# Performance work log

Hardware: AMD Instinct MI355X
Metric: run time of the kernel (lower is better)

Reference implementation:

```python
import jax, jax.numpy as jnp
import numpy as np

VOCAB, EMB, FEAT = 30000, 300, 2048
B, NQ, NW, NK = 256, 32, 12, 64


def setup_inputs() -> dict:
    key = jax.random.key(0)
    ks = jax.random.split(key, 10)
    return {
        "wv": jax.random.normal(ks[0], (VOCAB, EMB), jnp.float32),
        "Wf": jax.random.normal(ks[1], (EMB, FEAT), jnp.float32) * 0.02,
        "bf": jax.random.normal(ks[2], (EMB,), jnp.float32) * 0.02,
        "Wp": jax.random.normal(ks[3], (EMB, EMB), jnp.float32) * 0.05,
        "bp": jax.random.normal(ks[4], (EMB,), jnp.float32) * 0.02,
        "Wm": jax.random.normal(ks[5], (EMB, EMB), jnp.float32) * 0.05,
        "bm": jax.random.normal(ks[6], (EMB,), jnp.float32) * 0.02,
        "feature": jax.random.normal(ks[7], (B, NK, FEAT), jnp.float32),
        "query": jax.random.randint(ks[8], (B, NQ, NW), 0, VOCAB),
        "label": jax.random.randint(ks[9], (B, NK), 0, VOCAB),
    }


def reference(wv, Wf, bf, Wp, bp, Wm, bm, feature, query, label):
    # Dropouts act as identity in eval mode.
    eps = 1e-5
    q_emb = wv[query]                                   # [B, queries, words, D]
    k_emb = wv[label] + feature @ Wf.T + bf             # [B, objects, D]
    scale = 1.0 / np.sqrt(EMB)
    att = jnp.einsum('byqd,bkd->byqk', q_emb, k_emb) * scale
    att = jax.nn.softmax(att, axis=-1)                  # over objects
    q_max_att = jnp.max(att, axis=3)                    # [B, queries, words]
    neg_inf = -jnp.finfo(q_max_att.dtype).max
    q_max_att = jnp.where(query == 0, neg_inf, q_max_att)
    q_max_norm_att = jax.nn.softmax(q_max_att, axis=-1) / 5.0
    p_emb = jnp.einsum('byq,byqd->byd', q_max_norm_att, q_emb)  # [B, queries, D]
    p_emb = (p_emb @ Wp.T + bp) + eps * (p_emb @ Wm.T + bm)
    return p_emb, k_emb
```

## Files before the change

kernel.cpp:

```cpp
#include <hip/hip_runtime.h>

typedef unsigned short u16;
typedef unsigned int u32;
typedef __bf16 bf16x8 __attribute__((ext_vector_type(8)));
typedef float f32x4 __attribute__((ext_vector_type(4)));

#if defined(__has_builtin)
#  if __has_builtin(__builtin_amdgcn_cvt_pk_bf16_f32)
#    define PK_BF16 1
#  endif
#endif

__device__ __forceinline__ u16 f2bu(float f){
  u32 u = __float_as_uint(f);
  return (u16)((u + 0x7fffu + ((u >> 16) & 1u)) >> 16);
}
__device__ __forceinline__ float b2f(u16 u){
  union { float f; u32 i; } v; v.i = ((u32)u) << 16; return v.f;
}
__device__ __forceinline__ u32 pkbf(float a, float b){
#ifdef PK_BF16
  typedef __bf16 bf16x2 __attribute__((ext_vector_type(2)));
  union { bf16x2 h; u32 u; } c;
  c.h = __builtin_amdgcn_cvt_pk_bf16_f32(a, b);
  return c.u;
#else
  return (u32)f2bu(a) | ((u32)f2bu(b) << 16);
#endif
}
__device__ __forceinline__ void glds16(const u16* g, u16* l){
  __builtin_amdgcn_global_load_lds(
      (const __attribute__((address_space(1))) void*)g,
      (__attribute__((address_space(3))) void*)l, 16, 0, 0);
}
__device__ __forceinline__ void glds16f(const float* g, float* l){
  __builtin_amdgcn_global_load_lds(
      (const __attribute__((address_space(1))) void*)g,
      (__attribute__((address_space(3))) void*)l, 16, 0, 0);
}

__global__ __launch_bounds__(256) void prep_wc(
    const float* __restrict__ Wp, const float* __restrict__ bp,
    const float* __restrict__ Wm, const float* __restrict__ bm,
    u16* __restrict__ Wc, float* __restrict__ bc)
{
  int idx = blockIdx.x * 256 + threadIdx.x;
  if (idx < 384 * 160) {
    int n = idx / 160, k = (idx % 160) * 2;
    float v0 = 0.f, v1 = 0.f;
    if (n < 300 && k < 300) {
      v0 = Wp[n * 300 + k]     + 1e-5f * Wm[n * 300 + k];
      v1 = Wp[n * 300 + k + 1] + 1e-5f * Wm[n * 300 + k + 1];
    }
    ((u32*)Wc)[idx] = pkbf(v0, v1);
    if (idx < 384) bc[idx] = (idx < 300) ? bp[idx] + 1e-5f * bm[idx] : 0.f;
  }
}

__global__ __launch_bounds__(256) void prep_wv16(
    const float* __restrict__ wv, u16* __restrict__ wv16)
{
  int idx = blockIdx.x * 256 + threadIdx.x;
  if (idx < 30000 * 160) {
    int row = idx / 160, k = (idx % 160) * 2;
    float v0 = 0.f, v1 = 0.f;
    if (k < 300) {
      v0 = wv[(size_t)row * 300 + k];
      v1 = wv[(size_t)row * 300 + k + 1];
    }
    ((u32*)wv16)[idx] = pkbf(v0, v1);
  }
}

__global__ __launch_bounds__(256) void prep_wf16(
    const float* __restrict__ Wf, u16* __restrict__ Wf16)
{
  int i = blockIdx.x * 256 + threadIdx.x;
  if (i < 384 * 1024) {
    int row = i >> 10, c2 = (i & 1023) * 2;
    float v0 = 0.f, v1 = 0.f;
    if (row < 300) {
      v0 = Wf[(size_t)row * 2048 + c2];
      v1 = Wf[(size_t)row * 2048 + c2 + 1];
    }
    ((u32*)Wf16)[i] = pkbf(v0, v1);
  }
}

template <int GLDS>
__global__ __launch_bounds__(256) void gemm0_kernel(
    const float* __restrict__ A, const float* __restrict__ B,
    const u16* __restrict__ Af16, const u16* __restrict__ Bf16,
    const float* __restrict__ bias,
    const int* __restrict__ label, const float* __restrict__ wv,
    float* __restrict__ C, u16* __restrict__ kemb16)
{
  __shared__ __align__(16) u16 As[128 * 32];
  __shared__ __align__(16) u16 Bs[128 * 32];
  const int lda = 2048, K = 2048, nbn = 3, nsrc = 300;
  int t = threadIdx.x;
  int bm = (blockIdx.x / nbn) * 128;
  int bn = (blockIdx.x % nbn) * 128;
  int lane = t & 63, w = t >> 6;
  int wm = (w >> 1) * 64, wn = (w & 1) * 64;

  f32x4 acc[4][4];
  for (int i = 0; i < 4; i++)
    for (int j = 0; j < 4; j++)
      for (int r = 0; r < 4; r++) acc[i][j][r] = 0.f;

  int mrow = lane & 15, q = lane >> 4;

  for (int kk = 0; kk < K; kk += 32) {
    #pragma unroll
    for (int p = 0; p < 2; p++) {
      int idx = t + p * 256;
      int row = idx >> 2, ch = idx & 3;
      int brow = bn + row;
      if (brow >= nsrc) brow = 0;
      const float4* ap = (const float4*)&A[(size_t)(bm + row) * lda + kk + ch * 8];
      float4 a0 = ap[0], a1 = ap[1];
      const float4* bpp = (const float4*)&B[(size_t)brow * lda + kk + ch * 8];
      float4 b0 = bpp[0], b1 = bpp[1];
      union { u32 u[4]; uint4 v; } pa, pb;
      pa.u[0] = pkbf(a0.x, a0.y); pa.u[1] = pkbf(a0.z, a0.w);
      pa.u[2] = pkbf(a1.x, a1.y); pa.u[3] = pkbf(a1.z, a1.w);
      pb.u[0] = pkbf(b0.x, b0.y); pb.u[1] = pkbf(b0.z, b0.w);
      pb.u[2] = pkbf(b1.x, b1.y); pb.u[3] = pkbf(b1.z, b1.w);
      *(uint4*)&As[idx * 8] = pa.v;
      *(uint4*)&Bs[idx * 8] = pb.v;
    }
    __syncthreads();

    bf16x8 af[4], bfr[4];
    #pragma unroll
    for (int i = 0; i < 4; i++)
      af[i] = *(const bf16x8*)&As[(wm + i * 16 + mrow) * 32 + q * 8];
    #pragma unroll
    for (int j = 0; j < 4; j++)
      bfr[j] = *(const bf16x8*)&Bs[(wn + j * 16 + mrow) * 32 + q * 8];
    #pragma unroll
    for (int i = 0; i < 4; i++)
      #pragma unroll
      for (int j = 0; j < 4; j++)
        acc[i][j] = __builtin_amdgcn_mfma_f32_16x16x32_bf16(
            af[i], bfr[j], acc[i][j], 0, 0, 0);
    __syncthreads();
  }

  #pragma unroll
  for (int i = 0; i < 4; i++)
    #pragma unroll
    for (int j = 0; j < 4; j++) {
      int col = bn + wn + j * 16 + (lane & 15);
      int rb = bm + wm + i * 16 + (lane >> 4) * 4;
      #pragma unroll
      for (int r = 0; r < 4; r++) {
        int m = rb + r;
        if (col < 300) {
          float v = acc[i][j][r];
          v += bias[col] + wv[(size_t)label[m] * 300 + col];
          C[(size_t)m * 300 + col] = v;
          if (kemb16) kemb16[(size_t)m * 320 + col] = f2bu(v);
        } else if (kemb16 && col < 320) {
          kemb16[(size_t)m * 320 + col] = 0;
        }
      }
    }
}

__global__ __launch_bounds__(64) void gemm0v5_kernel(
    const float* __restrict__ A, const u16* __restrict__ Bf16,
    const float* __restrict__ bias, const int* __restrict__ label,
    const float* __restrict__ wv, float* __restrict__ C,
    u16* __restrict__ kemb16)
{
  __shared__ __align__(16) float As[2][64 * 32];
  __shared__ __align__(16) u16  Bs[2][64 * 32];
  int lane = threadIdx.x;
  int g = blockIdx.x;
  int xcd = g & 7, loc = g >> 3;
  int mloc = loc / 5, nn = loc % 5;
  int bm = (xcd * 32 + mloc) * 64;
  int bn = nn * 64;
  int mrow = lane & 15, q = lane >> 4;

  f32x4 acc[4][4];
  #pragma unroll
  for (int i = 0; i < 4; i++)
    #pragma unroll
    for (int j = 0; j < 4; j++)
      #pragma unroll
      for (int r = 0; r < 4; r++) acc[i][j][r] = 0.f;

  int rlA = lane >> 3, chA = lane & 7;
  int rlB = lane >> 2, chB = lane & 3;
  const float* gA = &A[(size_t)(bm + rlA) * 2048 + ((chA ^ rlA) << 2)];
  const u16*   gB = &Bf16[(size_t)(bn + rlB) * 2048 + (chB << 3)];

#define STAGE_V5(buf, kk) do {                                          \
    _Pragma("unroll")                                                   \
    for (int p = 0; p < 8; p++)                                         \
      glds16f(gA + (size_t)p * 8 * 2048 + (kk), &As[buf][(p * 8) * 32]);\
    _Pragma("unroll")                                                   \
    for (int p = 0; p < 4; p++)                                         \
      glds16(gB + (size_t)p * 16 * 2048 + (kk), &Bs[buf][(p * 16) * 32]);\
  } while (0)

  STAGE_V5(0, 0);

  for (int it = 0; it < 64; ++it) {
    int cur = it & 1;
    if (it < 63) {
      STAGE_V5(cur ^ 1, (it + 1) * 32);
      asm volatile("s_waitcnt vmcnt(12)" ::: "memory");
    } else {
      asm volatile("s_waitcnt vmcnt(0)" ::: "memory");
    }
    __builtin_amdgcn_sched_barrier(0);

    bf16x8 af[4], bfr[4];
    #pragma unroll
    for (int i = 0; i < 4; i++) {
      int r = i * 16 + mrow;
      int c0 = ((2 * q) ^ (r & 7)) * 4;
      int c1 = ((2 * q + 1) ^ (r & 7)) * 4;
      f32x4 x = *(const f32x4*)&As[cur][r * 32 + c0];
      f32x4 y = *(const f32x4*)&As[cur][r * 32 + c1];
      union { u32 u[4]; bf16x8 h; } cc;
      cc.u[0] = pkbf(x[0], x[1]); cc.u[1] = pkbf(x[2], x[3]);
      cc.u[2] = pkbf(y[0], y[1]); cc.u[3] = pkbf(y[2], y[3]);
      af[i] = cc.h;
    }
    #pragma unroll
    for (int j = 0; j < 4; j++)
      bfr[j] = *(const bf16x8*)&Bs[cur][(j * 16 + mrow) * 32 + q * 8];
    #pragma unroll
    for (int i = 0; i < 4; i++)
      #pragma unroll
      for (int j = 0; j < 4; j++)
        acc[i][j] = __builtin_amdgcn_mfma_f32_16x16x32_bf16(
            af[i], bfr[j], acc[i][j], 0, 0, 0);
  }
#undef STAGE_V5

  #pragma unroll
  for (int i = 0; i < 4; i++)
    #pragma unroll
    for (int j = 0; j < 4; j++) {
      int col = bn + j * 16 + (lane & 15);
      int rb = bm + i * 16 + (lane >> 4) * 4;
      #pragma unroll
      for (int r = 0; r < 4; r++) {
        int m = rb + r;
        if (col < 300) {
          float v = acc[i][j][r] + bias[col] + wv[(size_t)label[m] * 300 + col];
          C[(size_t)m * 300 + col] = v;
          kemb16[(size_t)m * 320 + col] = f2bu(v);
        } else {
          kemb16[(size_t)m * 320 + col] = 0;
        }
      }
    }
}

#define KES 344
template <int FULL>
__global__ __launch_bounds__(256) void attn_kernel(
    const float* __restrict__ wv, const u16* __restrict__ wv16,
    const int* __restrict__ query,
    const float* __restrict__ kout, const u16* __restrict__ kemb16,
    u16* __restrict__ praw)
{
  __shared__ __align__(16) u16 ke[64 * KES];
  __shared__ __align__(16) int qoff[192];
  __shared__ __align__(16) float awd[192];
  __shared__ __align__(16) float wt[192];

  int blk = blockIdx.x, b = blk >> 1, bh = blk & 1;
  int t = threadIdx.x;
  int lane = t & 63, w = t >> 6;

  if (FULL) {
    for (int i = t; i < 2560; i += 256) {
      int row = i / 40, ch = i % 40;
      *(uint4*)&ke[row * KES + ch * 8] =
          *(const uint4*)&kemb16[(size_t)(b * 64 + row) * 320 + ch * 8];
    }
  } else {
    for (int i = t; i < 4800; i += 256) {
      int row = i / 75, c4 = i % 75;
      float4 v = *(const float4*)&kout[(size_t)(b * 64 + row) * 300 + c4 * 4];
      *(u32*)&ke[row * KES + c4 * 4]     = pkbf(v.x, v.y);
      *(u32*)&ke[row * KES + c4 * 4 + 2] = pkbf(v.z, v.w);
    }
    for (int i = t; i < 640; i += 256) {
      int row = i / 10, c2 = i % 10;
      *(u32*)&ke[row * KES + 300 + c2 * 2] = 0;
    }
  }
  if (t < 192)
    qoff[t] = query[b * 384 + bh * 192 + t] * (FULL ? 320 : 300);
  __syncthreads();

  int mrow = lane & 15, q = lane >> 4;
  f32x4 acc[3][4];
  #pragma unroll
  for (int i = 0; i < 3; i++)
    #pragma unroll
    for (int j = 0; j < 4; j++)
      #pragma unroll
      for (int r = 0; r < 4; r++) acc[i][j][r] = 0.f;

  int base[3];
  #pragma unroll
  for (int i = 0; i < 3; i++) base[i] = qoff[w * 48 + i * 16 + mrow];
  int keb = mrow * KES + q * 8;

  bf16x8 afn[3];
  #pragma unroll
  for (int i = 0; i < 3; i++) {
    if (FULL)
      afn[i] = *(const bf16x8*)&wv16[(size_t)base[i] + q * 8];
  }

  for (int k0 = 0; k0 < 320; k0 += 32) {
    bf16x8 af[3], bfr[4];
    #pragma unroll
    for (int i = 0; i < 3; i++) {
      if (FULL) {
        af[i] = afn[i];
        if (k0 + 32 < 320)
          afn[i] = *(const bf16x8*)&wv16[(size_t)base[i] + k0 + 32 + q * 8];
      } else {
        int cs = k0 + q * 8;
        union { u32 u[4]; bf16x8 h; } c;
        if (cs + 8 <= 300) {
          const float4* p = (const float4*)&wv[(size_t)base[i] + cs];
          float4 x = p[0], y = p[1];
          c.u[0] = pkbf(x.x, x.y); c.u[1] = pkbf(x.z, x.w);
          c.u[2] = pkbf(y.x, y.y); c.u[3] = pkbf(y.z, y.w);
        } else if (cs < 300) {
          float4 x = *(const float4*)&wv[(size_t)base[i] + 296];
          c.u[0] = pkbf(x.x, x.y); c.u[1] = pkbf(x.z, x.w);
          c.u[2] = 0; c.u[3] = 0;
        } else {
          c.u[0] = 0; c.u[1] = 0; c.u[2] = 0; c.u[3] = 0;
        }
        af[i] = c.h;
      }
    }
    #pragma unroll
    for (int j = 0; j < 4; j++)
      bfr[j] = *(const bf16x8*)&ke[j * 16 * KES + keb + k0];
    #pragma unroll
    for (int i = 0; i < 3; i++)
      #pragma unroll
      for (int j = 0; j < 4; j++)
        acc[i][j] = __builtin_amdgcn_mfma_f32_16x16x32_bf16(
            af[i], bfr[j], acc[i][j], 0, 0, 0);
  }

  const float scale = 0.05773502691896258f;
  #pragma unroll
  for (int i = 0; i < 3; i++)
    #pragma unroll
    for (int r = 0; r < 4; r++) {
      float mx = fmaxf(fmaxf(acc[i][0][r], acc[i][1][r]),
                       fmaxf(acc[i][2][r], acc[i][3][r]));
      #pragma unroll
      for (int d = 1; d < 16; d <<= 1)
        mx = fmaxf(mx, __shfl_xor(mx, d));
      float se = 0.f;
      #pragma unroll
      for (int j = 0; j < 4; j++)
        se += __expf((acc[i][j][r] - mx) * scale);
      #pragma unroll
      for (int d = 1; d < 16; d <<= 1)
        se += __shfl_xor(se, d);
      if (mrow == 0) {
        int wl = w * 48 + i * 16 + q * 4 + r;
        awd[wl] = (qoff[wl] == 0) ? -3.402823466e38f : (1.0f / se);
      }
    }
  __syncthreads();

  if (t < 16) {
    int yb = t * 12;
    float m2 = -3.402823466e38f;
    for (int i = 0; i < 12; i++) m2 = fmaxf(m2, awd[yb + i]);
    float e[12], s2 = 0.f;
    for (int i = 0; i < 12; i++) { e[i] = __expf(awd[yb + i] - m2); s2 += e[i]; }
    float inv = 0.2f / s2;
    for (int i = 0; i < 12; i++) wt[yb + i] = e[i] * inv;
  }
  __syncthreads();

  #pragma unroll
  for (int yy = 0; yy < 4; yy++) {
    int yl = w * 4 + yy;
    int row = b * 32 + bh * 16 + yl;
    if (FULL) {
      if (lane < 40) {
        float s[8];
        #pragma unroll
        for (int e = 0; e < 8; e++) s[e] = 0.f;
        for (int i = 0; i < 12; i++) {
          float g = wt[yl * 12 + i];
          union { uint4 v; u16 h[8]; } qv;
          qv.v = *(const uint4*)&wv16[(size_t)qoff[yl * 12 + i] + lane * 8];
          #pragma unroll
          for (int e = 0; e < 8; e++) s[e] += g * b2f(qv.h[e]);
        }
        union { uint4 v; u16 h[8]; } o;
        #pragma unroll
        for (int e = 0; e < 8; e++) o.h[e] = f2bu(s[e]);
        *(uint4*)&praw[(size_t)row * 320 + lane * 8] = o.v;
      }
    } else {
      #pragma unroll
      for (int c = 0; c < 5; c++) {
        int d = c * 64 + lane;
        float s = 0.f;
        if (d < 300)
          for (int i = 0; i < 12; i++)
            s += wt[yl * 12 + i] * wv[(size_t)qoff[yl * 12 + i] + d];
        praw[(size_t)row * 320 + d] = f2bu(s);
      }
    }
  }
}

__global__ __launch_bounds__(256) void proj_kernel(
    const u16* __restrict__ praw, const u16* __restrict__ Wc,
    const float* __restrict__ bc, float* __restrict__ P)
{
  __shared__ __align__(16) u16 As[128 * 32];
  __shared__ __align__(16) u16 Bs[128 * 32];
  int t = threadIdx.x;
  int bm = (blockIdx.x / 3) * 128;
  int bn = (blockIdx.x % 3) * 128;
  int lane = t & 63, w = t >> 6;
  int wm = (w >> 1) * 64, wn = (w & 1) * 64;

  f32x4 acc[4][4];
  for (int i = 0; i < 4; i++)
    for (int j = 0; j < 4; j++)
      for (int r = 0; r < 4; r++) acc[i][j][r] = 0.f;

  int mrow = lane & 15, q = lane >> 4;

  for (int kk = 0; kk < 320; kk += 32) {
    int r0 = w * 32;
    int rl = lane >> 2, ch = lane & 3;
    #pragma unroll
    for (int p = 0; p < 2; p++) {
      int row = r0 + p * 16 + rl;
      glds16(&praw[(size_t)(bm + row) * 320 + kk + ch * 8],
             &As[(r0 + p * 16) * 32]);
      glds16(&Wc[(size_t)(bn + row) * 320 + kk + ch * 8],
             &Bs[(r0 + p * 16) * 32]);
    }
    __syncthreads();

    bf16x8 af[4], bfr[4];
    #pragma unroll
    for (int i = 0; i < 4; i++)
      af[i] = *(const bf16x8*)&As[(wm + i * 16 + mrow) * 32 + q * 8];
    #pragma unroll
    for (int j = 0; j < 4; j++)
      bfr[j] = *(const bf16x8*)&Bs[(wn + j * 16 + mrow) * 32 + q * 8];
    #pragma unroll
    for (int i = 0; i < 4; i++)
      #pragma unroll
      for (int j = 0; j < 4; j++)
        acc[i][j] = __builtin_amdgcn_mfma_f32_16x16x32_bf16(
            af[i], bfr[j], acc[i][j], 0, 0, 0);
    __syncthreads();
  }

  #pragma unroll
  for (int i = 0; i < 4; i++)
    #pragma unroll
    for (int j = 0; j < 4; j++) {
      int col = bn + wn + j * 16 + (lane & 15);
      if (col >= 300) continue;
      int rb = bm + wm + i * 16 + (lane >> 4) * 4;
      #pragma unroll
      for (int r = 0; r < 4; r++)
        P[(size_t)(rb + r) * 300 + col] = acc[i][j][r] + bc[col];
    }
}

extern "C" void kernel_launch(void* const* d_in, const int* in_sizes, int n_in,
                              void* d_out, int out_size, void* d_ws,
                              size_t ws_size, hipStream_t stream)
{
  const float* wv      = (const float*)d_in[0];
  const float* Wf      = (const float*)d_in[1];
  const float* bf      = (const float*)d_in[2];
  const float* Wp      = (const float*)d_in[3];
  const float* bp      = (const float*)d_in[4];
  const float* Wm      = (const float*)d_in[5];
  const float* bm      = (const float*)d_in[6];
  const float* feature = (const float*)d_in[7];
  const int*   query   = (const int*)d_in[8];
  const int*   label   = (const int*)d_in[9];

  float* out   = (float*)d_out;
  float* p_out = out;
  float* k_out = out + 2457600;

  char* ws = (char*)d_ws;
  int t2 = ws_size >= (size_t)103857664;
  int t1 = ws_size >= (size_t)35175936;
  u16 *wf16 = 0, *wv16 = 0, *kemb16 = 0, *praw, *Wc;
  float* bc;
  if (t2) {
    wv16   = (u16*)(ws + 67108864);
    kemb16 = (u16*)(ws + 86308864);
    praw   = (u16*)(ws + 96794624);
    Wc     = (u16*)(ws + 102037504);
    wf16   = (u16*)(ws + 102283264);
    bc     = (float*)(ws + 103856128);
  } else if (t1) {
    wv16   = (u16*)ws;
    kemb16 = (u16*)(ws + 19200000);
    praw   = (u16*)(ws + 29685760);
    Wc     = (u16*)(ws + 34928640);
    bc     = (float*)(ws + 35174400);
  } else {
    praw   = (u16*)ws;
    Wc     = (u16*)(ws + 5242880);
    bc     = (float*)(ws + 5488640);
  }

  prep_wc<<<240, 256, 0, stream>>>(Wp, bp, Wm, bm, Wc, bc);
  if (t1 || t2)
    prep_wv16<<<18750, 256, 0, stream>>>(wv, wv16);
  if (t2) {
    prep_wf16<<<1536, 256, 0, stream>>>(Wf, wf16);
    gemm0v5_kernel<<<1280, 64, 0, stream>>>(feature, wf16, bf,
                                            label, wv, k_out, kemb16);
  } else {
    gemm0_kernel<0><<<384, 256, 0, stream>>>(feature, Wf, 0, 0, bf,
                                             label, wv, k_out, kemb16);
  }

  if (t1 || t2)
    attn_kernel<1><<<512, 256, 0, stream>>>(wv, wv16, query, k_out,
                                            kemb16, praw);
  else
    attn_kernel<0><<<512, 256, 0, stream>>>(wv, wv16, query, k_out,
                                            kemb16, praw);

  proj_kernel<<<192, 256, 0, stream>>>(praw, Wc, bc, p_out);
}
```

Before: 366.9 us.

## Switch feature GEMM to 128x128 split-K tiles with separate reduction kernel

Replaces the single-wave 64x64 double-buffered GEMM with a 4-wave 128x128 tile kernel that splits K into three chunks, writing fp32 partials to workspace. A new reduce kernel sums the partials and adds the bias and label embedding, then writes k_out and the bf16 padded copy. The aim is more reuse per block and better occupancy and load balance across the 1152 blocks. In exchange it drops the double buffering, so each K step waits on its loads behind a barrier, and it adds about 59 MB of partial-sum traffic plus an extra launch. The partial buffer sits at workspace offset 0, which is also not used by the t2 layout.

```diff
diff --git a/kernel.cpp b/kernel.cpp
--- a/kernel.cpp
+++ b/kernel.cpp
@@ -169,20 +169,22 @@
     }
 }
 
-__global__ __launch_bounds__(64) void gemm0v5_kernel(
+__global__ __launch_bounds__(256) void gemm0v6_kernel(
     const float* __restrict__ A, const u16* __restrict__ Bf16,
-    const float* __restrict__ bias, const int* __restrict__ label,
-    const float* __restrict__ wv, float* __restrict__ C,
-    u16* __restrict__ kemb16)
-{
-  __shared__ __align__(16) float As[2][64 * 32];
-  __shared__ __align__(16) u16  Bs[2][64 * 32];
-  int lane = threadIdx.x;
+    float* __restrict__ P3)
+{
+  __shared__ __align__(16) float As[128 * 32];
+  __shared__ __align__(16) u16  Bs[128 * 32];
+  int t = threadIdx.x;
+  int lane = t & 63, w = t >> 6;
   int g = blockIdx.x;
-  int xcd = g & 7, loc = g >> 3;
-  int mloc = loc / 5, nn = loc % 5;
-  int bm = (xcd * 32 + mloc) * 64;
-  int bn = nn * 64;
+  int xcd = g & 7, seq = g >> 3;
+  int mloc = seq / 9, rem = seq % 9;
+  int nn = rem % 3, kc = rem / 3;
+  int bm = (xcd * 16 + mloc) * 128;
+  int bn = nn * 128;
+  int k0 = kc * 672, kend = (kc == 2) ? 2048 : k0 + 672;
+  int wm = (w >> 1) * 64, wn = (w & 1) * 64;
   int mrow = lane & 15, q = lane >> 4;
 
   f32x4 acc[4][4];
@@ -195,38 +197,28 @@
 
   int rlA = lane >> 3, chA = lane & 7;
   int rlB = lane >> 2, chB = lane & 3;
-  const float* gA = &A[(size_t)(bm + rlA) * 2048 + ((chA ^ rlA) << 2)];
-  const u16*   gB = &Bf16[(size_t)(bn + rlB) * 2048 + (chB << 3)];
-
-#define STAGE_V5(buf, kk) do {                                          \
-    _Pragma("unroll")                                                   \
-    for (int p = 0; p < 8; p++)                                         \
-      glds16f(gA + (size_t)p * 8 * 2048 + (kk), &As[buf][(p * 8) * 32]);\
-    _Pragma("unroll")                                                   \
-    for (int p = 0; p < 4; p++)                                         \
-      glds16(gB + (size_t)p * 16 * 2048 + (kk), &Bs[buf][(p * 16) * 32]);\
-  } while (0)
-
-  STAGE_V5(0, 0);
-
-  for (int it = 0; it < 64; ++it) {
-    int cur = it & 1;
-    if (it < 63) {
-      STAGE_V5(cur ^ 1, (it + 1) * 32);
-      asm volatile("s_waitcnt vmcnt(12)" ::: "memory");
-    } else {
-      asm volatile("s_waitcnt vmcnt(0)" ::: "memory");
-    }
-    __builtin_amdgcn_sched_barrier(0);
+  const float* gA = &A[(size_t)(bm + w * 32 + rlA) * 2048 + ((chA ^ rlA) << 2)];
+  const u16*   gB = &Bf16[(size_t)(bn + w * 32 + rlB) * 2048 + (chB << 3)];
+  float* lA = &As[(w * 32) * 32];
+  u16*   lB = &Bs[(w * 32) * 32];
+
+  for (int kk = k0; kk < kend; kk += 32) {
+    #pragma unroll
+    for (int p = 0; p < 4; p++)
+      glds16f(gA + (size_t)p * 8 * 2048 + kk, lA + p * 8 * 32);
+    #pragma unroll
+    for (int p = 0; p < 2; p++)
+      glds16(gB + (size_t)p * 16 * 2048 + kk, lB + p * 16 * 32);
+    __syncthreads();
 
     bf16x8 af[4], bfr[4];
     #pragma unroll
     for (int i = 0; i < 4; i++) {
-      int r = i * 16 + mrow;
+      int r = wm + i * 16 + mrow;
       int c0 = ((2 * q) ^ (r & 7)) * 4;
       int c1 = ((2 * q + 1) ^ (r & 7)) * 4;
-      f32x4 x = *(const f32x4*)&As[cur][r * 32 + c0];
-      f32x4 y = *(const f32x4*)&As[cur][r * 32 + c1];
+      f32x4 x = *(const f32x4*)&As[r * 32 + c0];
+      f32x4 y = *(const f32x4*)&As[r * 32 + c1];
       union { u32 u[4]; bf16x8 h; } cc;
       cc.u[0] = pkbf(x[0], x[1]); cc.u[1] = pkbf(x[2], x[3]);
       cc.u[2] = pkbf(y[0], y[1]); cc.u[3] = pkbf(y[2], y[3]);
@@ -234,34 +226,59 @@
     }
     #pragma unroll
     for (int j = 0; j < 4; j++)
-      bfr[j] = *(const bf16x8*)&Bs[cur][(j * 16 + mrow) * 32 + q * 8];
+      bfr[j] = *(const bf16x8*)&Bs[(wn + j * 16 + mrow) * 32 + q * 8];
     #pragma unroll
     for (int i = 0; i < 4; i++)
       #pragma unroll
       for (int j = 0; j < 4; j++)
         acc[i][j] = __builtin_amdgcn_mfma_f32_16x16x32_bf16(
             af[i], bfr[j], acc[i][j], 0, 0, 0);
-  }
-#undef STAGE_V5
+    __syncthreads();
+  }
 
   #pragma unroll
   for (int i = 0; i < 4; i++)
     #pragma unroll
     for (int j = 0; j < 4; j++) {
-      int col = bn + j * 16 + (lane & 15);
-      int rb = bm + i * 16 + (lane >> 4) * 4;
-      #pragma unroll
-      for (int r = 0; r < 4; r++) {
-        int m = rb + r;
-        if (col < 300) {
-          float v = acc[i][j][r] + bias[col] + wv[(size_t)label[m] * 300 + col];
-          C[(size_t)m * 300 + col] = v;
-          kemb16[(size_t)m * 320 + col] = f2bu(v);
-        } else {
-          kemb16[(size_t)m * 320 + col] = 0;
-        }
-      }
-    }
+      int col = bn + wn + j * 16 + (lane & 15);
+      if (col >= 300) continue;
+      int rb = bm + wm + i * 16 + (lane >> 4) * 4;
+      #pragma unroll
+      for (int r = 0; r < 4; r++)
+        P3[(size_t)kc * 4915200 + (size_t)(rb + r) * 300 + col] = acc[i][j][r];
+    }
+}
+
+__global__ __launch_bounds__(256) void reduce_kernel(
+    const float* __restrict__ P3, const float* __restrict__ bf,
+    const int* __restrict__ label, const float* __restrict__ wv,
+    float* __restrict__ C, u16* __restrict__ kemb16)
+{
+  int idx = blockIdx.x * 256 + threadIdx.x;
+  if (idx >= 16384 * 80) return;
+  int m = idx / 80, c4 = idx % 80;
+  if (c4 < 75) {
+    int c = c4 * 4;
+    float4 a = *(const float4*)&P3[(size_t)m * 300 + c];
+    float4 b = *(const float4*)&P3[(size_t)4915200 + (size_t)m * 300 + c];
+    float4 d = *(const float4*)&P3[(size_t)9830400 + (size_t)m * 300 + c];
+    float4 wvv = *(const float4*)&wv[(size_t)label[m] * 300 + c];
+    float4 bfv = *(const float4*)&bf[c];
+    float4 v;
+    v.x = a.x + b.x + d.x + bfv.x + wvv.x;
+    v.y = a.y + b.y + d.y + bfv.y + wvv.y;
+    v.z = a.z + b.z + d.z + bfv.z + wvv.z;
+    v.w = a.w + b.w + d.w + bfv.w + wvv.w;
+    *(float4*)&C[(size_t)m * 300 + c] = v;
+    union { u16 h[4]; uint2 u; } o;
+    o.h[0] = f2bu(v.x); o.h[1] = f2bu(v.y);
+    o.h[2] = f2bu(v.z); o.h[3] = f2bu(v.w);
+    *(uint2*)&kemb16[(size_t)m * 320 + c] = o.u;
+  } else {
+    int c = 300 + (c4 - 75) * 4;
+    uint2 z; z.x = 0; z.y = 0;
+    *(uint2*)&kemb16[(size_t)m * 320 + c] = z;
+  }
 }
 
 #define KES 344
@@ -516,6 +533,7 @@
   int t1 = ws_size >= (size_t)35175936;
   u16 *wf16 = 0, *wv16 = 0, *kemb16 = 0, *praw, *Wc;
   float* bc;
+  float* P3 = (float*)ws;
   if (t2) {
     wv16   = (u16*)(ws + 67108864);
     kemb16 = (u16*)(ws + 86308864);
@@ -540,8 +558,9 @@
     prep_wv16<<<18750, 256, 0, stream>>>(wv, wv16);
   if (t2) {
     prep_wf16<<<1536, 256, 0, stream>>>(Wf, wf16);
-    gemm0v5_kernel<<<1280, 64, 0, stream>>>(feature, wf16, bf,
-                                            label, wv, k_out, kemb16);
+    gemm0v6_kernel<<<1152, 256, 0, stream>>>(feature, wf16, P3);
+    reduce_kernel<<<5120, 256, 0, stream>>>(P3, bf, label, wv,
+                                            k_out, kemb16);
   } else {
     gemm0_kernel<0><<<384, 256, 0, stream>>>(feature, Wf, 0, 0, bf,
                                              label, wv, k_out, kemb16);
```

Measured after the change: 369.0 us. No clear change (+0.6%).
